# Optimization experiments

Hardware: AMD Instinct MI355X
Metric: run time of the kernel (lower is better)

The kernel has to match this reference:

```python
import jax, jax.numpy as jnp
import numpy as np

HIST_BINS = 64
VMAX = 255.0


def setup_inputs() -> dict:
    key = jax.random.key(0)
    k0, k1, k2, k3, k4 = jax.random.split(key, 5)
    B, H, W = 128, 512, 512
    grad_map = jax.random.uniform(k0, (B, H, W), dtype=jnp.float32) * VMAX
    # torch default init scale ~ U(-1/sqrt(fan_in), 1/sqrt(fan_in)); plain normals are fine for a reference
    W1 = jax.random.normal(k1, (32, HIST_BINS), dtype=jnp.float32) * (1.0 / np.sqrt(HIST_BINS))
    b1 = jax.random.normal(k2, (32,), dtype=jnp.float32) * 0.01
    W2 = jax.random.normal(k3, (128, 32), dtype=jnp.float32) * (1.0 / np.sqrt(32))
    b2 = jax.random.normal(k4, (128,), dtype=jnp.float32) * 0.01
    return {"grad_map": grad_map, "W1": W1, "b1": b1, "W2": W2, "b2": b2}


def _histc(vals, weights):
    # torch.histc semantics: values outside [0, VMAX] ignored; value == VMAX lands in last bin
    idx = jnp.clip(jnp.floor(vals * (HIST_BINS / VMAX)).astype(jnp.int32), 0, HIST_BINS - 1)
    return jnp.bincount(idx, weights=weights, length=HIST_BINS)


def reference(grad_map, W1, b1, W2, b2):
    B = grad_map.shape[0]
    flat = grad_map.reshape(B, -1)                      # [B, N]
    valid = ((flat >= 0.0) & (flat <= VMAX)).astype(jnp.float32)
    hists = jax.vmap(_histc)(flat, valid)               # [B, HIST_BINS]
    # F.normalize(p=1): x / max(||x||_1, 1e-12)
    hists = hists / jnp.maximum(jnp.sum(jnp.abs(hists), axis=-1, keepdims=True), 1e-12)
    h = jax.nn.relu(hists @ W1.T + b1)                  # [B, 32]
    return h @ W2.T + b2                                # [B, output_dim]
```

## Files before the change

### kernel.cpp

```cpp
#include <hip/hip_runtime.h>

#define HIST_BINS 64
#define NBATCH 128
#define THREADS 256
#define BLOCKS_PER_BATCH 16
#define WAVES_PER_BLOCK (THREADS / 64)

__global__ __launch_bounds__(THREADS) void hist_kernel(
    const float* __restrict__ g, unsigned int* __restrict__ hist, int n_per_batch) {
    __shared__ unsigned int lh[WAVES_PER_BLOCK][HIST_BINS];

    const int tid  = threadIdx.x;
    const int wave = tid >> 6;

    for (int i = tid; i < WAVES_PER_BLOCK * HIST_BINS; i += THREADS)
        ((unsigned int*)lh)[i] = 0u;
    __syncthreads();

    const int batch = blockIdx.y;
    const float4* gp = (const float4*)(g + (size_t)batch * (size_t)n_per_batch);
    const int n4 = n_per_batch >> 2;
    const float scale = 64.0f / 255.0f;

    for (int i = blockIdx.x * THREADS + tid; i < n4; i += BLOCKS_PER_BATCH * THREADS) {
        float4 v = gp[i];
        float vs[4] = {v.x, v.y, v.z, v.w};
#pragma unroll
        for (int j = 0; j < 4; ++j) {
            float val = vs[j];
            if (val >= 0.0f && val <= 255.0f) {
                int idx = (int)floorf(val * scale);
                idx = min(max(idx, 0), HIST_BINS - 1);
                atomicAdd(&lh[wave][idx], 1u);
            }
        }
    }
    __syncthreads();

    if (tid < HIST_BINS) {
        unsigned int s = 0;
#pragma unroll
        for (int w = 0; w < WAVES_PER_BLOCK; ++w) s += lh[w][tid];
        atomicAdd(&hist[batch * HIST_BINS + tid], s);
    }
}

__global__ __launch_bounds__(128) void mlp_kernel(
    const unsigned int* __restrict__ hist,
    const float* __restrict__ W1, const float* __restrict__ b1,
    const float* __restrict__ W2, const float* __restrict__ b2,
    float* __restrict__ out) {
    __shared__ float hn[HIST_BINS];
    __shared__ float h[32];

    const int b   = blockIdx.x;
    const int tid = threadIdx.x;

    if (tid < HIST_BINS) hn[tid] = (float)hist[b * HIST_BINS + tid];
    __syncthreads();

    float sum = 0.0f;
    for (int i = 0; i < HIST_BINS; ++i) sum += hn[i];
    const float denom = fmaxf(sum, 1e-12f);
    __syncthreads();

    if (tid < HIST_BINS) hn[tid] = hn[tid] / denom;
    __syncthreads();

    if (tid < 32) {
        float acc = b1[tid];
        for (int k = 0; k < HIST_BINS; ++k) acc += hn[k] * W1[tid * HIST_BINS + k];
        h[tid] = fmaxf(acc, 0.0f);
    }
    __syncthreads();

    float acc = b2[tid];
    for (int k = 0; k < 32; ++k) acc += h[k] * W2[tid * 32 + k];
    out[b * 128 + tid] = acc;
}

extern "C" void kernel_launch(void* const* d_in, const int* in_sizes, int n_in,
                              void* d_out, int out_size, void* d_ws, size_t ws_size,
                              hipStream_t stream) {
    const float* g  = (const float*)d_in[0];
    const float* W1 = (const float*)d_in[1];
    const float* b1 = (const float*)d_in[2];
    const float* W2 = (const float*)d_in[3];
    const float* b2 = (const float*)d_in[4];
    float* out = (float*)d_out;

    unsigned int* hist = (unsigned int*)d_ws;
    const int n_per_batch = in_sizes[0] / NBATCH;

    hipMemsetAsync(hist, 0, NBATCH * HIST_BINS * sizeof(unsigned int), stream);

    hist_kernel<<<dim3(BLOCKS_PER_BATCH, NBATCH), THREADS, 0, stream>>>(g, hist, n_per_batch);
    mlp_kernel<<<NBATCH, 128, 0, stream>>>(hist, W1, b1, W2, b2, out);
}
```

Measured before the change: 198.7 us.

## Replace LDS atomics with per-thread packed 16-bit private histograms

Each thread now keeps its own histogram in LDS, packed as two 16-bit counters per word and laid out column-wise by thread, so updates are bank-conflict-free plain adds instead of contended shared atomics. Invalid values go to a dummy word so the update is branch-free. A tree reduction across threads merges the private histograms before one global atomic per bin. Blocks per batch are halved and each block reads a contiguous chunk with an unrolled loop. This trades a 33 KB LDS footprint per block, which lowers occupancy, plus an extra reduction phase, for removing atomic contention.

Result: slower. 206.0 us (+3.7%).

```diff
diff --git a/kernel.cpp b/kernel.cpp
--- a/kernel.cpp
+++ b/kernel.cpp
@@ -3,45 +3,54 @@
 #define HIST_BINS 64
 #define NBATCH 128
 #define THREADS 256
-#define BLOCKS_PER_BATCH 16
-#define WAVES_PER_BLOCK (THREADS / 64)
+#define BLOCKS_PER_BATCH 8
+#define WORDS 32
 
 __global__ __launch_bounds__(THREADS) void hist_kernel(
     const float* __restrict__ g, unsigned int* __restrict__ hist, int n_per_batch) {
-    __shared__ unsigned int lh[WAVES_PER_BLOCK][HIST_BINS];
+    __shared__ unsigned int lh[WORDS + 1][THREADS];
 
-    const int tid  = threadIdx.x;
-    const int wave = tid >> 6;
+    const int tid = threadIdx.x;
 
-    for (int i = tid; i < WAVES_PER_BLOCK * HIST_BINS; i += THREADS)
-        ((unsigned int*)lh)[i] = 0u;
+#pragma unroll
+    for (int w = 0; w < WORDS + 1; ++w) lh[w][tid] = 0u;
     __syncthreads();
 
     const int batch = blockIdx.y;
-    const float4* gp = (const float4*)(g + (size_t)batch * (size_t)n_per_batch);
-    const int n4 = n_per_batch >> 2;
+    const int elems_per_block = n_per_batch / BLOCKS_PER_BATCH;
+    const float4* gp = (const float4*)(g + (size_t)batch * n_per_batch
+                                         + (size_t)blockIdx.x * elems_per_block);
+    const int n4 = elems_per_block >> 2;
     const float scale = 64.0f / 255.0f;
 
-    for (int i = blockIdx.x * THREADS + tid; i < n4; i += BLOCKS_PER_BATCH * THREADS) {
+#pragma unroll 4
+    for (int i = tid; i < n4; i += THREADS) {
         float4 v = gp[i];
         float vs[4] = {v.x, v.y, v.z, v.w};
 #pragma unroll
         for (int j = 0; j < 4; ++j) {
             float val = vs[j];
-            if (val >= 0.0f && val <= 255.0f) {
-                int idx = (int)floorf(val * scale);
-                idx = min(max(idx, 0), HIST_BINS - 1);
-                atomicAdd(&lh[wave][idx], 1u);
-            }
+            int bin = (int)floorf(val * scale);
+            bin = min(max(bin, 0), HIST_BINS - 1);
+            bool valid = (val >= 0.0f) && (val <= 255.0f);
+            int w = valid ? (bin >> 1) : WORDS;
+            lh[w][tid] += 1u << ((bin & 1) << 4);
         }
     }
     __syncthreads();
 
+    for (int s = THREADS / 2; s >= 1; s >>= 1) {
+        if (tid < s) {
+#pragma unroll
+            for (int w = 0; w < WORDS; ++w) lh[w][tid] += lh[w][tid + s];
+        }
+        __syncthreads();
+    }
+
     if (tid < HIST_BINS) {
-        unsigned int s = 0;
-#pragma unroll
-        for (int w = 0; w < WAVES_PER_BLOCK; ++w) s += lh[w][tid];
-        atomicAdd(&hist[batch * HIST_BINS + tid], s);
+        unsigned int v = lh[tid >> 1][0];
+        unsigned int c = (v >> ((tid & 1) << 4)) & 0xFFFFu;
+        atomicAdd(&hist[batch * HIST_BINS + tid], c);
     }
 }
 
```
